# Optimization experiments

Hardware: AMD Instinct MI355X
Metric: run time of the kernel (lower is better)

## Reference

```python
import jax, jax.numpy as jnp
import numpy as np

HIDDEN = 768
HEADS = 12
HEAD_DIM = HIDDEN // HEADS


def setup_inputs() -> dict:
    key = jax.random.key(0)
    ks = jax.random.split(key, 6)
    B, N = 32, 577  # N = 1 CLS + 576 patches
    x = jax.random.normal(ks[0], (B, N, HIDDEN), dtype=jnp.float32)
    seg_bias = jax.random.uniform(ks[1], (B, N - 1), dtype=jnp.float32)
    w_qkv = jax.random.normal(ks[2], (HIDDEN, 3 * HIDDEN), dtype=jnp.float32) * 0.02
    b_qkv = jnp.zeros((3 * HIDDEN,), dtype=jnp.float32)
    w_proj = jax.random.normal(ks[3], (HIDDEN, HIDDEN), dtype=jnp.float32) * 0.02
    b_proj = jnp.zeros((HIDDEN,), dtype=jnp.float32)
    seg_scale = jnp.ones((), dtype=jnp.float32)
    return {"x": x, "seg_bias": seg_bias, "w_qkv": w_qkv, "b_qkv": b_qkv,
            "w_proj": w_proj, "b_proj": b_proj, "seg_scale": seg_scale}


def reference(x, seg_bias, w_qkv, b_qkv, w_proj, b_proj, seg_scale):
    B, N, _ = x.shape
    scale = HEAD_DIM ** -0.5
    qkv = x @ w_qkv + b_qkv                       # (B, N, 3*H*D)
    qkv = qkv.reshape(B, N, 3, HEADS, HEAD_DIM)
    q = qkv[:, :, 0].transpose(0, 2, 1, 3)        # (B, H, N, D)
    k = qkv[:, :, 1].transpose(0, 2, 1, 3)
    v = qkv[:, :, 2].transpose(0, 2, 1, 3)
    attn = jnp.einsum('bhqd,bhkd->bhqk', q, k) * scale  # (B, H, N, N)
    # additive seg bias on CLS-query row, patch keys only (cols 1:)
    bias = (seg_bias * seg_scale)[:, None, None, :]     # (B,1,1,N-1)
    attn = attn.at[:, :, 0:1, 1:].add(bias)
    attn = jax.nn.softmax(attn, axis=-1)
    out = jnp.einsum('bhqk,bhkd->bhqd', attn, v)        # (B, H, N, D)
    out = out.transpose(0, 2, 1, 3).reshape(B, N, HIDDEN)
    return out @ w_proj + b_proj
```

## Files before the change

kernel.cpp:

```cpp
#include <hip/hip_runtime.h>


typedef unsigned short bf16_t;
typedef __attribute__((ext_vector_type(8))) short short8;
typedef __attribute__((ext_vector_type(4))) float f32x4;

#define B_    32
#define N_    577
#define BN_   18464
#define HID_  768
#define NH_   12
#define HD_   64
#define QKVC_ 2304
#define NPAD_ 640

__device__ __forceinline__ bf16_t f2bf(float f) {
  union { float f; unsigned u; } x; x.f = f;
  unsigned r = x.u + 0x7fffu + ((x.u >> 16) & 1u);
  return (bf16_t)(r >> 16);
}

__global__ __launch_bounds__(256) void cast_kernel(const float* __restrict__ in,
                                                   bf16_t* __restrict__ out, int n4) {
  int i = blockIdx.x * 256 + threadIdx.x;
  if (i >= n4) return;
  float4 v = ((const float4*)in)[i];
  ushort4 o;
  o.x = f2bf(v.x); o.y = f2bf(v.y); o.z = f2bf(v.z); o.w = f2bf(v.w);
  ((ushort4*)out)[i] = o;
}

__global__ __launch_bounds__(256) void transpose_cast_kernel(const float* __restrict__ in,
                                                             bf16_t* __restrict__ out,
                                                             int R, int C) {
  __shared__ float tile[32][33];
  int c0 = blockIdx.x * 32, r0 = blockIdx.y * 32;
  int tx = threadIdx.x, ty = threadIdx.y;
  #pragma unroll
  for (int i = ty; i < 32; i += 8)
    tile[i][tx] = in[(size_t)(r0 + i) * C + c0 + tx];
  __syncthreads();
  #pragma unroll
  for (int i = ty; i < 32; i += 8)
    out[(size_t)(c0 + i) * R + r0 + tx] = f2bf(tile[tx][i]);
}

template <int OUT_BF16>
__global__ __launch_bounds__(256, 3) void gemm_bf16_kernel(
    const bf16_t* __restrict__ A,
    const bf16_t* __restrict__ Bt,
    const float* __restrict__ bias,
    void* __restrict__ Cout,
    int M, int Nc) {
  __shared__ bf16_t As[128 * 64];
  __shared__ bf16_t Bs[128 * 64];

  const int tid  = threadIdx.x;
  const int lane = tid & 63, w = tid >> 6;
  const int quad = lane >> 4, l16 = lane & 15;

  const int Mb = (M + 127) >> 7;
  const int Nb = Nc >> 7;
  const int np_full = Mb >> 3;
  const int rem = Mb - np_full * 8;
  int bid = blockIdx.x;
  int m_blk, n_blk;
  int body = np_full * 8 * Nb;
  if (bid < body) {
    int p = bid / (8 * Nb), local = bid % (8 * Nb);
    m_blk = p * 8 + (local & 7);
    n_blk = local >> 3;
  } else {
    int t = bid - body;
    m_blk = np_full * 8 + t % rem;
    n_blk = t / rem;
  }
  const int m0 = m_blk * 128, n0 = n_blk * 128;
  const int wm = (w >> 1) * 64, wn = (w & 1) * 64;

  f32x4 acc[4][4];
  #pragma unroll
  for (int i = 0; i < 4; ++i)
    #pragma unroll
    for (int j = 0; j < 4; ++j)
      acc[i][j] = (f32x4){0.f, 0.f, 0.f, 0.f};

  for (int kt = 0; kt < 768; kt += 64) {
    __syncthreads();
    #pragma unroll
    for (int it = 0; it < 4; ++it) {
      int gi = it * 256 + tid;
      int row = gi >> 3, chp = gi & 7;
      int ch = chp ^ (row & 7);
      int gm = m0 + row; if (gm >= M) gm = M - 1;
      __builtin_amdgcn_global_load_lds(
          (const __attribute__((address_space(1))) unsigned int*)(A + (size_t)gm * 768 + kt + ch * 8),
          (__attribute__((address_space(3))) unsigned int*)(As + gi * 8),
          16, 0, 0);
      int gn = n0 + row;
      __builtin_amdgcn_global_load_lds(
          (const __attribute__((address_space(1))) unsigned int*)(Bt + (size_t)gn * 768 + kt + ch * 8),
          (__attribute__((address_space(3))) unsigned int*)(Bs + gi * 8),
          16, 0, 0);
    }
    __syncthreads();

    #pragma unroll
    for (int ks = 0; ks < 2; ++ks) {
      short8 af[4], bfr[4];
      #pragma unroll
      for (int i = 0; i < 4; ++i) {
        int row = wm + i * 16 + l16;
        int c = ks * 4 + quad;
        af[i] = *(const short8*)(As + row * 64 + (c ^ (row & 7)) * 8);
      }
      #pragma unroll
      for (int j = 0; j < 4; ++j) {
        int row = wn + j * 16 + l16;
        int c = ks * 4 + quad;
        bfr[j] = *(const short8*)(Bs + row * 64 + (c ^ (row & 7)) * 8);
      }
      #pragma unroll
      for (int i = 0; i < 4; ++i)
        #pragma unroll
        for (int j = 0; j < 4; ++j)
          acc[i][j] = __builtin_amdgcn_mfma_f32_16x16x32_bf16(af[i], bfr[j], acc[i][j], 0, 0, 0);
    }
  }

  #pragma unroll
  for (int i = 0; i < 4; ++i) {
    int mrow_base = m0 + wm + i * 16 + quad * 4;
    #pragma unroll
    for (int j = 0; j < 4; ++j) {
      int col = n0 + wn + j * 16 + l16;
      float bs = bias[col];
      #pragma unroll
      for (int r = 0; r < 4; ++r) {
        int row = mrow_base + r;
        if (row < M) {
          float v = acc[i][j][r] + bs;
          if (OUT_BF16)
            ((bf16_t*)Cout)[(size_t)row * Nc + col] = f2bf(v);
          else
            ((float*)Cout)[(size_t)row * Nc + col] = v;
        }
      }
    }
  }
}

__global__ __launch_bounds__(256) void vt_kernel(const bf16_t* __restrict__ qkv,
                                                 bf16_t* __restrict__ vT) {
  const int t = blockIdx.x, h = blockIdx.y, b = blockIdx.z;
  const int tid = threadIdx.x;
  __shared__ bf16_t Ls[64 * 65];
  const int kv0 = t * 64;
  const bf16_t* Vp = qkv + (size_t)b * N_ * QKVC_ + 2 * HID_ + h * HD_;

  #pragma unroll
  for (int it = 0; it < 2; ++it) {
    int idx = it * 256 + tid;
    int row = idx >> 3, ch = idx & 7;
    int krow = kv0 + row; if (krow > N_ - 1) krow = N_ - 1;
    short8 v8 = *(const short8*)(Vp + (size_t)krow * QKVC_ + ch * 8);
    #pragma unroll
    for (int j = 0; j < 8; ++j)
      Ls[(ch * 8 + j) * 65 + row] = (bf16_t)v8[j];
  }
  __syncthreads();
  bf16_t* outp = vT + ((size_t)(b * NH_ + h) * HD_) * NPAD_;
  #pragma unroll
  for (int it = 0; it < 2; ++it) {
    int idx = it * 256 + tid;
    int d = idx >> 3, kc = idx & 7;
    short8 o8;
    #pragma unroll
    for (int j = 0; j < 8; ++j)
      o8[j] = (short)Ls[d * 65 + kc * 8 + j];
    *(short8*)(outp + (size_t)d * NPAD_ + kv0 + kc * 8) = o8;
  }
}

__global__ __launch_bounds__(256) void attn_kernel(
    const bf16_t* __restrict__ qkv,
    const bf16_t* __restrict__ vT,
    const float* __restrict__ seg_bias,
    const float* __restrict__ seg_scale,
    bf16_t* __restrict__ out) {
  const int bid  = blockIdx.x;
  const int pair = bid % (B_ * NH_);
  const int qt   = bid / (B_ * NH_);
  const int h    = pair % NH_;
  const int b    = pair / NH_;
  const int tid = threadIdx.x;
  const int w = tid >> 6, lane = tid & 63;
  const int quad = lane >> 4, l16 = lane & 15;

  __shared__ bf16_t Ks[2][64 * 72];
  __shared__ bf16_t Vt[2][64 * 72];
  __shared__ bf16_t Pb[4][32 * 72];

  const bf16_t* Qbase = qkv + (size_t)b * N_ * QKVC_ + h * HD_;
  const bf16_t* Kbase = Qbase + HID_;
  const bf16_t* Vtb   = vT + ((size_t)(b * NH_ + h) * HD_) * NPAD_;

  const int q0 = qt * 128 + w * 32;
  short8 qf[2][2];
  #pragma unroll
  for (int mi = 0; mi < 2; ++mi) {
    int qr = q0 + mi * 16 + l16;
    if (qr > N_ - 1) qr = N_ - 1;
    qf[mi][0] = *(const short8*)(Qbase + (size_t)qr * QKVC_ + quad * 8);
    qf[mi][1] = *(const short8*)(Qbase + (size_t)qr * QKVC_ + 32 + quad * 8);
  }
  const float qsc = 0.125f * 1.44269504f;
  #pragma unroll
  for (int mi = 0; mi < 2; ++mi)
    #pragma unroll
    for (int c = 0; c < 2; ++c)
      #pragma unroll
      for (int j = 0; j < 8; ++j) {
        unsigned u = ((unsigned)(unsigned short)qf[mi][c][j]) << 16;
        union { unsigned u; float f; } x; x.u = u;
        qf[mi][c][j] = (short)f2bf(x.f * qsc);
      }

  f32x4 o[2][4];
  float lsum[2][4];
  #pragma unroll
  for (int mi = 0; mi < 2; ++mi)
    #pragma unroll
    for (int j = 0; j < 4; ++j) {
      o[mi][j] = (f32x4){0.f, 0.f, 0.f, 0.f};
      lsum[mi][j] = 0.f;
    }

  const float ssl = seg_scale[0] * 1.44269504f;
  const bool bias_wave = (qt == 0 && w == 0);
  bf16_t* pw = Pb[w];

  const int srow = tid >> 3;
  const int sch  = tid & 7;

  short8 kpre[2], vpre[2];
  #pragma unroll
  for (int it = 0; it < 2; ++it) {
    int row = it * 32 + srow;
    int krow = row; if (krow > N_ - 1) krow = N_ - 1;
    kpre[it] = *(const short8*)(Kbase + (size_t)krow * QKVC_ + sch * 8);
    vpre[it] = *(const short8*)(Vtb + (size_t)row * NPAD_ + sch * 8);
  }
  #pragma unroll
  for (int it = 0; it < 2; ++it) {
    int row = it * 32 + srow;
    *(short8*)(&Ks[0][0] + row * 72 + sch * 8) = kpre[it];
    *(short8*)(&Vt[0][0] + row * 72 + sch * 8) = vpre[it];
  }
  __syncthreads();

  for (int t = 0; t < 10; ++t) {
    const int cur = t & 1;
    const int kv0 = t * 64;
    const bf16_t* ks = &Ks[cur][0];
    const bf16_t* vt = &Vt[cur][0];

    if (t < 9) {
      const int kv1 = kv0 + 64;
      #pragma unroll
      for (int it = 0; it < 2; ++it) {
        int row = it * 32 + srow;
        int krow = kv1 + row; if (krow > N_ - 1) krow = N_ - 1;
        kpre[it] = *(const short8*)(Kbase + (size_t)krow * QKVC_ + sch * 8);
        vpre[it] = *(const short8*)(Vtb + (size_t)row * NPAD_ + kv1 + sch * 8);
      }
    }

    f32x4 s[2][4];
    #pragma unroll
    for (int mi = 0; mi < 2; ++mi)
      #pragma unroll
      for (int sub = 0; sub < 4; ++sub)
        s[mi][sub] = (f32x4){0.f, 0.f, 0.f, 0.f};
    #pragma unroll
    for (int sub = 0; sub < 4; ++sub) {
      short8 k0 = *(const short8*)(ks + (sub * 16 + l16) * 72 + quad * 8);
      short8 k1 = *(const short8*)(ks + (sub * 16 + l16) * 72 + 32 + quad * 8);
      #pragma unroll
      for (int mi = 0; mi < 2; ++mi) {
        s[mi][sub] = __builtin_amdgcn_mfma_f32_16x16x32_bf16(qf[mi][0], k0, s[mi][sub], 0, 0, 0);
        s[mi][sub] = __builtin_amdgcn_mfma_f32_16x16x32_bf16(qf[mi][1], k1, s[mi][sub], 0, 0, 0);
      }
    }

    if (bias_wave && quad == 0) {
      #pragma unroll
      for (int sub = 0; sub < 4; ++sub) {
        int key = kv0 + sub * 16 + l16;
        if (key >= 1 && key < N_)
          s[0][sub][0] += seg_bias[b * (N_ - 1) + key - 1] * ssl;
      }
    }

    #pragma unroll
    for (int mi = 0; mi < 2; ++mi)
      #pragma unroll
      for (int sub = 0; sub < 4; ++sub) {
        #pragma unroll
        for (int r = 0; r < 4; ++r) {
          float p = exp2f(s[mi][sub][r]);
          if (t == 9) {
            int key = kv0 + sub * 16 + l16;
            if (key >= N_) p = 0.f;
          }
          lsum[mi][r] += p;
          union { float f; unsigned u; } c; c.f = p;
          pw[(mi * 16 + r * 4 + quad) * 72 + sub * 16 + l16] =
              (bf16_t)((c.u + 0x8000u) >> 16);
        }
      }

    #pragma unroll
    for (int mi = 0; mi < 2; ++mi) {
      int prow = mi * 16 + ((l16 & 3) << 2) + (l16 >> 2);
      short8 pa0 = *(const short8*)(pw + prow * 72 + quad * 8);
      short8 pa1 = *(const short8*)(pw + prow * 72 + 32 + quad * 8);
      #pragma unroll
      for (int ds = 0; ds < 4; ++ds) {
        short8 vb0 = *(const short8*)(vt + (ds * 16 + l16) * 72 + quad * 8);
        short8 vb1 = *(const short8*)(vt + (ds * 16 + l16) * 72 + 32 + quad * 8);
        o[mi][ds] = __builtin_amdgcn_mfma_f32_16x16x32_bf16(pa0, vb0, o[mi][ds], 0, 0, 0);
        o[mi][ds] = __builtin_amdgcn_mfma_f32_16x16x32_bf16(pa1, vb1, o[mi][ds], 0, 0, 0);
      }
    }

    if (t < 9) {
      bf16_t* ksn = &Ks[1 - cur][0];
      bf16_t* vtn = &Vt[1 - cur][0];
      #pragma unroll
      for (int it = 0; it < 2; ++it) {
        int row = it * 32 + srow;
        *(short8*)(ksn + row * 72 + sch * 8) = kpre[it];
        *(short8*)(vtn + row * 72 + sch * 8) = vpre[it];
      }
    }
    __syncthreads();
  }

  #pragma unroll
  for (int mi = 0; mi < 2; ++mi)
    #pragma unroll
    for (int r = 0; r < 4; ++r) {
      float l = lsum[mi][r];
      #pragma unroll
      for (int off = 1; off < 16; off <<= 1)
        l += __shfl_xor(l, off);
      float inv = 1.0f / l;
      int row = q0 + mi * 16 + quad * 4 + r;
      if (row < N_) {
        size_t base = ((size_t)b * N_ + row) * HID_ + h * HD_;
        #pragma unroll
        for (int ds = 0; ds < 4; ++ds)
          out[base + ds * 16 + l16] = f2bf(o[mi][ds][r] * inv);
      }
    }
}

extern "C" void kernel_launch(void* const* d_in, const int* in_sizes, int n_in,
                              void* d_out, int out_size, void* d_ws, size_t ws_size,
                              hipStream_t stream) {
  const float* x         = (const float*)d_in[0];
  const float* seg_bias  = (const float*)d_in[1];
  const float* w_qkv     = (const float*)d_in[2];
  const float* b_qkv     = (const float*)d_in[3];
  const float* w_proj    = (const float*)d_in[4];
  const float* b_proj    = (const float*)d_in[5];
  const float* seg_scale = (const float*)d_in[6];

  char* ws = (char*)d_ws;
  bf16_t* xb     = (bf16_t*)ws;
  bf16_t* wqkvT  = (bf16_t*)(ws + 28360704);
  bf16_t* wprojT = (bf16_t*)(ws + 31899648);
  bf16_t* qkvb   = (bf16_t*)(ws + 33079296);
  bf16_t* vT     = (bf16_t*)(ws + 118161408);
  bf16_t* attnb  = xb;

  cast_kernel<<<(BN_ * HID_ / 4) / 256, 256, 0, stream>>>(x, xb, BN_ * HID_ / 4);
  dim3 tb(32, 8);
  transpose_cast_kernel<<<dim3(QKVC_ / 32, HID_ / 32), tb, 0, stream>>>(w_qkv, wqkvT, HID_, QKVC_);
  transpose_cast_kernel<<<dim3(HID_ / 32, HID_ / 32), tb, 0, stream>>>(w_proj, wprojT, HID_, HID_);

  gemm_bf16_kernel<1><<<145 * (QKVC_ / 128), 256, 0, stream>>>(
      xb, wqkvT, b_qkv, (void*)qkvb, BN_, QKVC_);

  vt_kernel<<<dim3(10, NH_, B_), 256, 0, stream>>>(qkvb, vT);

  attn_kernel<<<5 * NH_ * B_, 256, 0, stream>>>(qkvb, vT, seg_bias, seg_scale, attnb);

  gemm_bf16_kernel<0><<<145 * (HID_ / 128), 256, 0, stream>>>(
      attnb, wprojT, b_proj, d_out, BN_, HID_);
}
```

Baseline: 349.0 us.

## Permute V^T key order so P tiles store packed bf16 without transposed scatter

New measurement: 325.1 us. -6.9%, faster.

```diff
diff --git a/kernel.cpp b/kernel.cpp
--- a/kernel.cpp
+++ b/kernel.cpp
@@ -3,6 +3,7 @@
 
 typedef unsigned short bf16_t;
 typedef __attribute__((ext_vector_type(8))) short short8;
+typedef __attribute__((ext_vector_type(4))) short short4v;
 typedef __attribute__((ext_vector_type(4))) float f32x4;
 
 #define B_    32
@@ -13,11 +14,18 @@
 #define HD_   64
 #define QKVC_ 2304
 #define NPAD_ 640
+#define PB_LD 68
 
 __device__ __forceinline__ bf16_t f2bf(float f) {
   union { float f; unsigned u; } x; x.f = f;
   unsigned r = x.u + 0x7fffu + ((x.u >> 16) & 1u);
   return (bf16_t)(r >> 16);
+}
+
+__device__ __forceinline__ unsigned cvt_pk_bf16(float a, float b) {
+  unsigned r;
+  asm("v_cvt_pk_bf16_f32 %0, %1, %2" : "=v"(r) : "v"(a), "v"(b));
+  return r;
 }
 
 __global__ __launch_bounds__(256) void cast_kernel(const float* __restrict__ in,
@@ -176,8 +184,11 @@
     int d = idx >> 3, kc = idx & 7;
     short8 o8;
     #pragma unroll
-    for (int j = 0; j < 8; ++j)
-      o8[j] = (short)Ls[d * 65 + kc * 8 + j];
+    for (int j = 0; j < 8; ++j) {
+      int p = kc * 8 + j;
+      int ky = ((p & 3) << 4) | (p >> 2);
+      o8[j] = (short)Ls[d * 65 + ky];
+    }
     *(short8*)(outp + (size_t)d * NPAD_ + kv0 + kc * 8) = o8;
   }
 }
@@ -199,7 +210,7 @@
 
   __shared__ bf16_t Ks[2][64 * 72];
   __shared__ bf16_t Vt[2][64 * 72];
-  __shared__ bf16_t Pb[4][32 * 72];
+  __shared__ bf16_t Pb[4][32 * PB_LD];
 
   const bf16_t* Qbase = qkv + (size_t)b * N_ * QKVC_ + h * HD_;
   const bf16_t* Kbase = Qbase + HID_;
@@ -305,32 +316,38 @@
     #pragma unroll
     for (int mi = 0; mi < 2; ++mi)
       #pragma unroll
-      for (int sub = 0; sub < 4; ++sub) {
+      for (int r = 0; r < 4; ++r) {
+        float p[4];
         #pragma unroll
-        for (int r = 0; r < 4; ++r) {
-          float p = exp2f(s[mi][sub][r]);
+        for (int sub = 0; sub < 4; ++sub) {
+          float v = __builtin_amdgcn_exp2f(s[mi][sub][r]);
           if (t == 9) {
             int key = kv0 + sub * 16 + l16;
-            if (key >= N_) p = 0.f;
+            if (key >= N_) v = 0.f;
           }
-          lsum[mi][r] += p;
-          union { float f; unsigned u; } c; c.f = p;
-          pw[(mi * 16 + r * 4 + quad) * 72 + sub * 16 + l16] =
-              (bf16_t)((c.u + 0x8000u) >> 16);
+          lsum[mi][r] += v;
+          p[sub] = v;
         }
+        uint2 pk;
+        pk.x = cvt_pk_bf16(p[0], p[1]);
+        pk.y = cvt_pk_bf16(p[2], p[3]);
+        *(uint2*)(pw + (mi * 16 + quad * 4 + r) * PB_LD + l16 * 4) = pk;
       }
 
     #pragma unroll
     for (int mi = 0; mi < 2; ++mi) {
-      int prow = mi * 16 + ((l16 & 3) << 2) + (l16 >> 2);
-      short8 pa0 = *(const short8*)(pw + prow * 72 + quad * 8);
-      short8 pa1 = *(const short8*)(pw + prow * 72 + 32 + quad * 8);
+      const bf16_t* pr = pw + (mi * 16 + l16) * PB_LD + quad * 8;
+      union { short8 v; short4v h[2]; } pa0, pa1;
+      pa0.h[0] = *(const short4v*)(pr);
+      pa0.h[1] = *(const short4v*)(pr + 4);
+      pa1.h[0] = *(const short4v*)(pr + 32);
+      pa1.h[1] = *(const short4v*)(pr + 36);
       #pragma unroll
       for (int ds = 0; ds < 4; ++ds) {
         short8 vb0 = *(const short8*)(vt + (ds * 16 + l16) * 72 + quad * 8);
         short8 vb1 = *(const short8*)(vt + (ds * 16 + l16) * 72 + 32 + quad * 8);
-        o[mi][ds] = __builtin_amdgcn_mfma_f32_16x16x32_bf16(pa0, vb0, o[mi][ds], 0, 0, 0);
-        o[mi][ds] = __builtin_amdgcn_mfma_f32_16x16x32_bf16(pa1, vb1, o[mi][ds], 0, 0, 0);
+        o[mi][ds] = __builtin_amdgcn_mfma_f32_16x16x32_bf16(pa0.v, vb0, o[mi][ds], 0, 0, 0);
+        o[mi][ds] = __builtin_amdgcn_mfma_f32_16x16x32_bf16(pa1.v, vb1, o[mi][ds], 0, 0, 0);
       }
     }
 
```
